# Kernel optimization log

Hardware: AMD Instinct MI355X
Metric: run time of the kernel (lower is better)

## Reference

```python
import jax, jax.numpy as jnp
import numpy as np

B, S, D, H = 2, 2048, 1024, 16  # batch, seq, embed_dim, num_heads
DH = D // H                      # head dim = 64


def setup_inputs() -> dict:
    key = jax.random.key(0)
    kx, kq, kbq, kk, kbk, kv, kbv = jax.random.split(key, 7)
    scale = 1.0 / np.sqrt(D)
    return {
        "x": jax.random.normal(kx, (B, S, D), dtype=jnp.float32),
        "Wq": jax.random.normal(kq, (D, D), dtype=jnp.float32) * scale,
        "bq": jax.random.normal(kbq, (D,), dtype=jnp.float32) * 0.01,
        "Wk": jax.random.normal(kk, (D, D), dtype=jnp.float32) * scale,
        "bk": jax.random.normal(kbk, (D,), dtype=jnp.float32) * 0.01,
        "Wv": jax.random.normal(kv, (D, D), dtype=jnp.float32) * scale,
        "bv": jax.random.normal(kbv, (D,), dtype=jnp.float32) * 0.01,
    }


def reference(x, Wq, bq, Wk, bk, Wv, bv):
    # ooqkv_type == 'q', odeint_method == 'id': q branch = act(Linear(x)), exact GELU (torch nn.GELU default)
    q = jax.nn.gelu(x @ Wq + bq, approximate=False)
    k = x @ Wk + bk
    v = x @ Wv + bv
    # [B, S, D] -> [B, S, H, DH]
    q = q.reshape(B, S, H, DH)
    k = k.reshape(B, S, H, DH)
    v = v.reshape(B, S, H, DH)
    # NOTE: original module has NO 1/sqrt(d) scale — faithful reproduction
    att = jnp.einsum("bqhd,bkhd->bhqk", q, k)
    att = jax.nn.softmax(att, axis=-1)
    out = jnp.einsum("bhqk,bkhd->bqhd", att, v)
    return out.reshape(B, S, D)
```

## Files before the change

### kernel.cpp

```cpp
#include <hip/hip_runtime.h>
#include <math.h>

#define B_  2
#define S_  2048
#define D_  1024
#define H_  16
#define DH_ 64
#define M_  (B_ * S_)

typedef _Float16 half_t;
typedef __attribute__((ext_vector_type(8))) _Float16 h8;
typedef __attribute__((ext_vector_type(4))) _Float16 h4;
typedef __attribute__((ext_vector_type(4))) float   f32x4;

#define LOG2E 1.44269504088896f

__device__ __forceinline__ void gll16(const half_t* g, half_t* l) {
    __builtin_amdgcn_global_load_lds(
        (__attribute__((address_space(1))) const void*)g,
        (__attribute__((address_space(3))) void*)l, 16, 0, 0);
}

__global__ __launch_bounds__(256) void prep_k(
    const float* __restrict__ x, half_t* __restrict__ xh,
    const float* __restrict__ Wq, const float* __restrict__ Wk,
    const float* __restrict__ Wv, half_t* __restrict__ Wt)
{
    const int bx = blockIdx.x;
    if (bx < 2048) {
        const size_t i = ((size_t)bx * 256 + threadIdx.x) * 8;
        const float4 a = *(const float4*)(x + i);
        const float4 b = *(const float4*)(x + i + 4);
        h8 o;
        o[0] = (half_t)a.x; o[1] = (half_t)a.y; o[2] = (half_t)a.z; o[3] = (half_t)a.w;
        o[4] = (half_t)b.x; o[5] = (half_t)b.y; o[6] = (half_t)b.z; o[7] = (half_t)b.w;
        *(h8*)(xh + i) = o;
    } else {
        const int gb    = bx - 2048;
        const int which = gb >> 9;
        const float* __restrict__ W = (which == 0) ? Wq : (which == 1) ? Wk : Wv;
        half_t* __restrict__ T = Wt + (size_t)which * D_ * D_;
        const int gw   = (gb & 511) * 4 + (threadIdx.x >> 6);
        const int lane = threadIdx.x & 63;
        const int n    = (gw & 15) * 64 + lane;
        const int k0   = (gw >> 4) * 8;
        h8 o;
        #pragma unroll
        for (int t = 0; t < 8; ++t) o[t] = (half_t)W[(size_t)(k0 + t) * D_ + n];
        *(h8*)(T + (size_t)n * D_ + k0) = o;
    }
}

__global__ __launch_bounds__(512) void qkv_gemm_f16(
    const half_t* __restrict__ xh, const half_t* __restrict__ Wt,
    const float* __restrict__ bq, const float* __restrict__ bk,
    const float* __restrict__ bv,
    half_t* __restrict__ Qo, half_t* __restrict__ Ko, half_t* __restrict__ Vt)
{
    const int lin = blockIdx.y * 24 + blockIdx.x;
    const int swz = (lin & 7) * 96 + (lin >> 3);
    const int n0g = (swz % 24) * 128;
    const int m0  = (swz / 24) * 128;
    const int which = n0g >> 10;
    const int n0    = n0g & 1023;
    const half_t* __restrict__ Wp  = Wt + (size_t)which * D_ * D_;
    const float* __restrict__ bias = (which == 0) ? bq : (which == 1) ? bk : bv;

    const int tid = threadIdx.x, lane = tid & 63, wave = tid >> 6;
    const int wm = (wave & 3) * 32, wn = (wave >> 2) * 64;
    const int ln = lane & 15, quad = lane >> 4;

    __shared__ __align__(16) half_t SMEM[128 * 136];
    half_t* const As = SMEM;
    half_t* const Bs = SMEM + 128 * 64;

    const int r0  = tid >> 3, c0 = tid & 7;
    const int cs  = c0 ^ (r0 & 7);
    const half_t* aS = xh + (size_t)(m0 + r0) * D_ + cs * 8;
    const half_t* bS = Wp + (size_t)(n0 + r0) * D_ + cs * 8;

    f32x4 acc[2][4];
    #pragma unroll
    for (int i = 0; i < 2; ++i)
        #pragma unroll
        for (int j = 0; j < 4; ++j) acc[i][j] = (f32x4){0.f, 0.f, 0.f, 0.f};

    for (int k0 = 0; k0 < D_; k0 += 64) {
        __syncthreads();
        gll16(aS,            &As[tid * 8]);
        gll16(aS + 64 * D_,  &As[(tid + 512) * 8]);
        gll16(bS,            &Bs[tid * 8]);
        gll16(bS + 64 * D_,  &Bs[(tid + 512) * 8]);
        aS += 64; bS += 64;
        __syncthreads();

        #pragma unroll
        for (int kc = 0; kc < 2; ++kc) {
            h8 af[2], bf[4];
            #pragma unroll
            for (int i = 0; i < 2; ++i) {
                const int r = wm + i * 16 + ln;
                af[i] = *(const h8*)&As[r * 64 + (((kc << 2) + quad) ^ (r & 7)) * 8];
            }
            #pragma unroll
            for (int j = 0; j < 4; ++j) {
                const int r = wn + j * 16 + ln;
                bf[j] = *(const h8*)&Bs[r * 64 + (((kc << 2) + quad) ^ (r & 7)) * 8];
            }
            #pragma unroll
            for (int i = 0; i < 2; ++i)
                #pragma unroll
                for (int j = 0; j < 4; ++j)
                    acc[i][j] = __builtin_amdgcn_mfma_f32_16x16x32_f16(
                        af[i], bf[j], acc[i][j], 0, 0, 0);
        }
    }

    if (which == 2) {
        #pragma unroll
        for (int j = 0; j < 4; ++j) {
            const int col = n0 + wn + j * 16 + ln;
            const int h = col >> 6, d = col & 63;
            const float bb = bias[col];
            #pragma unroll
            for (int i = 0; i < 2; ++i) {
                const int sg = m0 + wm + i * 16 + quad * 4;
                const int b  = sg >> 11, srow = sg & 2047;
                h4 pv;
                #pragma unroll
                for (int r = 0; r < 4; ++r) pv[r] = (half_t)(acc[i][j][r] + bb);
                *(h4*)(Vt + (((size_t)(b * H_ + h) * DH_ + d) * S_ + srow)) = pv;
            }
        }
    } else {
        half_t* __restrict__ outp = (which == 0) ? Qo : Ko;
        __syncthreads();
        #pragma unroll
        for (int j = 0; j < 4; ++j) {
            const int col = wn + j * 16 + ln;
            const float bb = bias[n0 + col];
            #pragma unroll
            for (int i = 0; i < 2; ++i) {
                #pragma unroll
                for (int r = 0; r < 4; ++r) {
                    const int row = wm + i * 16 + quad * 4 + r;
                    float t = acc[i][j][r] + bb;
                    if (which == 0) {
                        const float u = t * fmaf(t * t, 0.0356774081f, 0.7978845608f);
                        const float e = __builtin_amdgcn_exp2f(u * -2.88539008178f);
                        t = t * __builtin_amdgcn_rcpf(1.0f + e) * LOG2E;
                    }
                    SMEM[row * 136 + col] = (half_t)t;
                }
            }
        }
        __syncthreads();
        const int cc = tid & 15;
        const int rr = tid >> 4;
        #pragma unroll
        for (int p = 0; p < 4; ++p) {
            const int row = p * 32 + rr;
            const h8 v = *(const h8*)&SMEM[row * 136 + cc * 8];
            *(h8*)(outp + (size_t)(m0 + row) * D_ + n0 + cc * 8) = v;
        }
    }
}

#define DEFER_THR 10.0f
#define ATTN_TILE(KS, VS)                                                     \
    do {                                                                      \
        f32x4 sa[4];                                                          \
        __builtin_amdgcn_s_setprio(1);                                        \
        _Pragma("unroll")                                                     \
        for (int j = 0; j < 4; ++j) {                                         \
            const int rK = j * 16 + ln;                                       \
            const h8 ka0 = *(const h8*)&KS[rK * 64 + ((quad)     ^ (rK & 7)) * 8]; \
            const h8 ka1 = *(const h8*)&KS[rK * 64 + ((quad + 4) ^ (rK & 7)) * 8]; \
            f32x4 t = (f32x4){0.f, 0.f, 0.f, 0.f};                            \
            t = __builtin_amdgcn_mfma_f32_16x16x32_f16(ka0, qa0, t, 0, 0, 0); \
            t = __builtin_amdgcn_mfma_f32_16x16x32_f16(ka1, qa1, t, 0, 0, 0); \
            sa[j] = t;                                                        \
        }                                                                     \
        __builtin_amdgcn_s_setprio(0);                                        \
        float mxa = sa[0][0];                                                 \
        _Pragma("unroll")                                                     \
        for (int j = 0; j < 4; ++j)                                           \
            _Pragma("unroll")                                                 \
            for (int r = 0; r < 4; ++r) mxa = fmaxf(mxa, sa[j][r]);           \
        mxa = fmaxf(mxa, __shfl_xor(mxa, 16, 64));                            \
        mxa = fmaxf(mxa, __shfl_xor(mxa, 32, 64));                            \
        if (__ballot(mxa > m_a + DEFER_THR)) {                                \
            const float mna = fmaxf(m_a, mxa);                                \
            const float ala = __builtin_amdgcn_exp2f(m_a - mna);              \
            m_a = mna;                                                        \
            float ra[4];                                                      \
            _Pragma("unroll")                                                 \
            for (int r = 0; r < 4; ++r) ra[r] = __shfl(ala, quad * 4 + r, 64);\
            _Pragma("unroll")                                                 \
            for (int r = 0; r < 4; ++r) {                                     \
                la[r] *= ra[r];                                               \
                _Pragma("unroll")                                             \
                for (int j = 0; j < 4; ++j) Oa[j][r] *= ra[r];                \
            }                                                                 \
        }                                                                     \
        _Pragma("unroll")                                                     \
        for (int j = 0; j < 4; ++j) {                                         \
            h4 pva;                                                           \
            _Pragma("unroll")                                                 \
            for (int r = 0; r < 4; ++r)                                       \
                pva[r] = (half_t)__builtin_amdgcn_exp2f(sa[j][r] - m_a);      \
            *(h4*)&QPs[wave * 16 + ln][j * 16 + quad * 4] = pva;              \
        }                                                                     \
        const h8 pa0 = *(const h8*)&QPs[wave * 16 + ln][quad * 8];            \
        const h8 pa1 = *(const h8*)&QPs[wave * 16 + ln][32 + quad * 8];       \
        __builtin_amdgcn_s_setprio(1);                                        \
        _Pragma("unroll")                                                     \
        for (int j = 0; j < 4; ++j) {                                         \
            const int rV = j * 16 + ln;                                       \
            const h8 vb0 = *(const h8*)&VS[rV * 64 + ((quad)     ^ (rV & 7)) * 8]; \
            const h8 vb1 = *(const h8*)&VS[rV * 64 + ((quad + 4) ^ (rV & 7)) * 8]; \
            Oa[j] = __builtin_amdgcn_mfma_f32_16x16x32_f16(pa0, vb0, Oa[j], 0, 0, 0); \
            Oa[j] = __builtin_amdgcn_mfma_f32_16x16x32_f16(pa1, vb1, Oa[j], 0, 0, 0); \
        }                                                                     \
        la = __builtin_amdgcn_mfma_f32_16x16x32_f16(pa0, ones8, la, 0, 0, 0); \
        la = __builtin_amdgcn_mfma_f32_16x16x32_f16(pa1, ones8, la, 0, 0, 0); \
        __builtin_amdgcn_s_setprio(0);                                        \
    } while (0)

__global__ __launch_bounds__(512) void attn_f16(
    const half_t* __restrict__ Q, const half_t* __restrict__ K,
    const half_t* __restrict__ Vt, float* __restrict__ out)
{
    const int tid  = threadIdx.x;
    const int lane = tid & 63;
    const int wave = tid >> 6;
    const int ln   = lane & 15;
    const int quad = lane >> 4;

    const int lin = blockIdx.y * 16 + blockIdx.x;
    const int swz = (lin & 7) * 64 + (lin >> 3);
    const int bh  = swz >> 4;
    const int b   = bh >> 4;
    const int h   = bh & 15;
    const int q0  = (swz & 15) * 128;

    const half_t* __restrict__ Qb  = Q  + (size_t)b * S_ * D_ + h * DH_;
    const half_t* __restrict__ Kb  = K  + (size_t)b * S_ * D_ + h * DH_;
    const half_t* __restrict__ Vtb = Vt + (size_t)bh * DH_ * S_;

    __shared__ __align__(16) half_t Ks0[64 * 64];
    __shared__ __align__(16) half_t Vs0[64 * 64];
    __shared__ __align__(16) half_t Ks1[64 * 64];
    __shared__ __align__(16) half_t Vs1[64 * 64];
    __shared__ __align__(16) half_t QPs[128][72];

    const int sr  = tid >> 3, sc0 = tid & 7;
    const int scs = sc0 ^ (sr & 7);
    const half_t* kS = Kb  + (size_t)sr * D_ + scs * 8;
    const half_t* vS = Vtb + (size_t)sr * S_ + scs * 8;
    half_t* const kD0 = &Ks0[tid * 8];
    half_t* const vD0 = &Vs0[tid * 8];
    half_t* const kD1 = &Ks1[tid * 8];
    half_t* const vD1 = &Vs1[tid * 8];

    gll16(kS, kD0); gll16(vS, vD0);
    kS += 64 * D_; vS += 64;

    #pragma unroll
    for (int l = 0; l < 2; ++l) {
        const int c = tid + l * 512;
        const int r = c >> 3, k8 = c & 7;
        *(h8*)&QPs[r][k8 * 8] = *(const h8*)(Qb + (size_t)(q0 + r) * D_ + k8 * 8);
    }
    __syncthreads();
    const h8 qa0 = *(const h8*)&QPs[wave * 16 + ln][quad * 8];
    const h8 qa1 = *(const h8*)&QPs[wave * 16 + ln][32 + quad * 8];

    h8 ones8;
    #pragma unroll
    for (int t = 0; t < 8; ++t) ones8[t] = (half_t)1.0f;

    f32x4 Oa[4];
    #pragma unroll
    for (int j = 0; j < 4; ++j) Oa[j] = (f32x4){0.f, 0.f, 0.f, 0.f};
    f32x4 la = (f32x4){0.f, 0.f, 0.f, 0.f};
    float m_a = -INFINITY;

    for (int it = 0; it < 16; ++it) {
        gll16(kS, kD1); gll16(vS, vD1);
        kS += 64 * D_; vS += 64;
        ATTN_TILE(Ks0, Vs0);
        __syncthreads();

        if (it < 15) {
            gll16(kS, kD0); gll16(vS, vD0);
            kS += 64 * D_; vS += 64;
        }
        ATTN_TILE(Ks1, Vs1);
        __syncthreads();
    }

    #pragma unroll
    for (int r = 0; r < 4; ++r) {
        const float iva = 1.0f / la[r];
        const int rowa = q0 + wave * 16 + quad * 4 + r;
        #pragma unroll
        for (int j = 0; j < 4; ++j)
            out[((size_t)b * S_ + rowa) * D_ + h * DH_ + j * 16 + ln] = Oa[j][r] * iva;
    }
}

extern "C" void kernel_launch(void* const* d_in, const int* in_sizes, int n_in,
                              void* d_out, int out_size, void* d_ws, size_t ws_size,
                              hipStream_t stream) {
    const float* x  = (const float*)d_in[0];
    const float* Wq = (const float*)d_in[1];
    const float* bq = (const float*)d_in[2];
    const float* Wk = (const float*)d_in[3];
    const float* bk = (const float*)d_in[4];
    const float* Wv = (const float*)d_in[5];
    const float* bv = (const float*)d_in[6];
    float* out = (float*)d_out;

    const size_t nmd = (size_t)M_ * D_;
    const size_t ndd = (size_t)D_ * D_;
    half_t* xh  = (half_t*)d_ws;
    half_t* Wt  = xh + nmd;
    half_t* Qh  = Wt + 3 * ndd;
    half_t* Kh  = Qh + nmd;
    half_t* Vtw = Kh + nmd;

    prep_k<<<2048 + 1536, 256, 0, stream>>>(x, xh, Wq, Wk, Wv, Wt);
    qkv_gemm_f16<<<dim3(3 * D_ / 128, M_ / 128), 512, 0, stream>>>(
        xh, Wt, bq, bk, bv, Qh, Kh, Vtw);
    attn_f16<<<dim3(S_ / 128, B_ * H_), 512, 0, stream>>>(Qh, Kh, Vtw, out);
}
```

Measured before the change: 168.8 us.

## Process two 16-row query tiles per wave in attention with 256-thread blocks

Each wave of the attention kernel now handles 32 query rows as two 16-row subtiles, and the block shrinks from 512 to 256 threads. Each K/V fragment read from LDS is reused for both subtiles, roughly halving LDS traffic per MFMA. The softmax statistics are tracked per subtile, and the K/V tile loads are split across fewer threads. The cost is more registers per wave and fewer waves per block to hide latency, which may lower occupancy.

```diff
diff --git a/kernel.cpp b/kernel.cpp
--- a/kernel.cpp
+++ b/kernel.cpp
@@ -169,7 +169,7 @@
 #define DEFER_THR 10.0f
 #define ATTN_TILE(KS, VS)                                                     \
     do {                                                                      \
-        f32x4 sa[4];                                                          \
+        f32x4 sa[4], sb[4];                                                   \
         __builtin_amdgcn_s_setprio(1);                                        \
         _Pragma("unroll")                                                     \
         for (int j = 0; j < 4; ++j) {                                         \
@@ -180,39 +180,60 @@
             t = __builtin_amdgcn_mfma_f32_16x16x32_f16(ka0, qa0, t, 0, 0, 0); \
             t = __builtin_amdgcn_mfma_f32_16x16x32_f16(ka1, qa1, t, 0, 0, 0); \
             sa[j] = t;                                                        \
+            f32x4 u = (f32x4){0.f, 0.f, 0.f, 0.f};                            \
+            u = __builtin_amdgcn_mfma_f32_16x16x32_f16(ka0, qc0, u, 0, 0, 0); \
+            u = __builtin_amdgcn_mfma_f32_16x16x32_f16(ka1, qc1, u, 0, 0, 0); \
+            sb[j] = u;                                                        \
         }                                                                     \
         __builtin_amdgcn_s_setprio(0);                                        \
-        float mxa = sa[0][0];                                                 \
+        float mxa = sa[0][0], mxb = sb[0][0];                                 \
         _Pragma("unroll")                                                     \
         for (int j = 0; j < 4; ++j)                                           \
             _Pragma("unroll")                                                 \
-            for (int r = 0; r < 4; ++r) mxa = fmaxf(mxa, sa[j][r]);           \
+            for (int r = 0; r < 4; ++r) {                                     \
+                mxa = fmaxf(mxa, sa[j][r]);                                   \
+                mxb = fmaxf(mxb, sb[j][r]);                                   \
+            }                                                                 \
         mxa = fmaxf(mxa, __shfl_xor(mxa, 16, 64));                            \
         mxa = fmaxf(mxa, __shfl_xor(mxa, 32, 64));                            \
-        if (__ballot(mxa > m_a + DEFER_THR)) {                                \
+        mxb = fmaxf(mxb, __shfl_xor(mxb, 16, 64));                            \
+        mxb = fmaxf(mxb, __shfl_xor(mxb, 32, 64));                            \
+        if (__ballot(mxa > m_a + DEFER_THR || mxb > m_b + DEFER_THR)) {       \
             const float mna = fmaxf(m_a, mxa);                                \
+            const float mnb = fmaxf(m_b, mxb);                                \
             const float ala = __builtin_amdgcn_exp2f(m_a - mna);              \
-            m_a = mna;                                                        \
-            float ra[4];                                                      \
-            _Pragma("unroll")                                                 \
-            for (int r = 0; r < 4; ++r) ra[r] = __shfl(ala, quad * 4 + r, 64);\
+            const float alb = __builtin_amdgcn_exp2f(m_b - mnb);              \
+            m_a = mna; m_b = mnb;                                             \
+            float ra[4], rb[4];                                               \
             _Pragma("unroll")                                                 \
             for (int r = 0; r < 4; ++r) {                                     \
-                la[r] *= ra[r];                                               \
+                ra[r] = __shfl(ala, quad * 4 + r, 64);                        \
+                rb[r] = __shfl(alb, quad * 4 + r, 64);                        \
+            }                                                                 \
+            _Pragma("unroll")                                                 \
+            for (int r = 0; r < 4; ++r) {                                     \
+                la[r] *= ra[r]; lb[r] *= rb[r];                               \
                 _Pragma("unroll")                                             \
-                for (int j = 0; j < 4; ++j) Oa[j][r] *= ra[r];                \
+                for (int j = 0; j < 4; ++j) {                                 \
+                    Oa[j][r] *= ra[r]; Ob[j][r] *= rb[r];                     \
+                }                                                             \
             }                                                                 \
         }                                                                     \
         _Pragma("unroll")                                                     \
         for (int j = 0; j < 4; ++j) {                                         \
-            h4 pva;                                                           \
+            h4 pva, pvb;                                                      \
             _Pragma("unroll")                                                 \
-            for (int r = 0; r < 4; ++r)                                       \
+            for (int r = 0; r < 4; ++r) {                                     \
                 pva[r] = (half_t)__builtin_amdgcn_exp2f(sa[j][r] - m_a);      \
-            *(h4*)&QPs[wave * 16 + ln][j * 16 + quad * 4] = pva;              \
+                pvb[r] = (half_t)__builtin_amdgcn_exp2f(sb[j][r] - m_b);      \
+            }                                                                 \
+            *(h4*)&QPs[wave * 32 + ln][j * 16 + quad * 4]      = pva;         \
+            *(h4*)&QPs[wave * 32 + 16 + ln][j * 16 + quad * 4] = pvb;         \
         }                                                                     \
-        const h8 pa0 = *(const h8*)&QPs[wave * 16 + ln][quad * 8];            \
-        const h8 pa1 = *(const h8*)&QPs[wave * 16 + ln][32 + quad * 8];       \
+        const h8 pa0 = *(const h8*)&QPs[wave * 32 + ln][quad * 8];            \
+        const h8 pa1 = *(const h8*)&QPs[wave * 32 + ln][32 + quad * 8];       \
+        const h8 pb0 = *(const h8*)&QPs[wave * 32 + 16 + ln][quad * 8];       \
+        const h8 pb1 = *(const h8*)&QPs[wave * 32 + 16 + ln][32 + quad * 8];  \
         __builtin_amdgcn_s_setprio(1);                                        \
         _Pragma("unroll")                                                     \
         for (int j = 0; j < 4; ++j) {                                         \
@@ -221,13 +242,17 @@
             const h8 vb1 = *(const h8*)&VS[rV * 64 + ((quad + 4) ^ (rV & 7)) * 8]; \
             Oa[j] = __builtin_amdgcn_mfma_f32_16x16x32_f16(pa0, vb0, Oa[j], 0, 0, 0); \
             Oa[j] = __builtin_amdgcn_mfma_f32_16x16x32_f16(pa1, vb1, Oa[j], 0, 0, 0); \
+            Ob[j] = __builtin_amdgcn_mfma_f32_16x16x32_f16(pb0, vb0, Ob[j], 0, 0, 0); \
+            Ob[j] = __builtin_amdgcn_mfma_f32_16x16x32_f16(pb1, vb1, Ob[j], 0, 0, 0); \
         }                                                                     \
         la = __builtin_amdgcn_mfma_f32_16x16x32_f16(pa0, ones8, la, 0, 0, 0); \
         la = __builtin_amdgcn_mfma_f32_16x16x32_f16(pa1, ones8, la, 0, 0, 0); \
+        lb = __builtin_amdgcn_mfma_f32_16x16x32_f16(pb0, ones8, lb, 0, 0, 0); \
+        lb = __builtin_amdgcn_mfma_f32_16x16x32_f16(pb1, ones8, lb, 0, 0, 0); \
         __builtin_amdgcn_s_setprio(0);                                        \
     } while (0)
 
-__global__ __launch_bounds__(512) void attn_f16(
+__global__ __launch_bounds__(256) void attn_f16(
     const half_t* __restrict__ Q, const half_t* __restrict__ K,
     const half_t* __restrict__ Vt, float* __restrict__ out)
 {
@@ -258,42 +283,53 @@
     const int scs = sc0 ^ (sr & 7);
     const half_t* kS = Kb  + (size_t)sr * D_ + scs * 8;
     const half_t* vS = Vtb + (size_t)sr * S_ + scs * 8;
-    half_t* const kD0 = &Ks0[tid * 8];
-    half_t* const vD0 = &Vs0[tid * 8];
-    half_t* const kD1 = &Ks1[tid * 8];
-    half_t* const vD1 = &Vs1[tid * 8];
-
-    gll16(kS, kD0); gll16(vS, vD0);
+
+    gll16(kS,           &Ks0[tid * 8]);
+    gll16(kS + 32 * D_, &Ks0[(tid + 256) * 8]);
+    gll16(vS,           &Vs0[tid * 8]);
+    gll16(vS + 32 * S_, &Vs0[(tid + 256) * 8]);
     kS += 64 * D_; vS += 64;
 
     #pragma unroll
-    for (int l = 0; l < 2; ++l) {
-        const int c = tid + l * 512;
+    for (int l = 0; l < 4; ++l) {
+        const int c = tid + l * 256;
         const int r = c >> 3, k8 = c & 7;
         *(h8*)&QPs[r][k8 * 8] = *(const h8*)(Qb + (size_t)(q0 + r) * D_ + k8 * 8);
     }
     __syncthreads();
-    const h8 qa0 = *(const h8*)&QPs[wave * 16 + ln][quad * 8];
-    const h8 qa1 = *(const h8*)&QPs[wave * 16 + ln][32 + quad * 8];
+    const h8 qa0 = *(const h8*)&QPs[wave * 32 + ln][quad * 8];
+    const h8 qa1 = *(const h8*)&QPs[wave * 32 + ln][32 + quad * 8];
+    const h8 qc0 = *(const h8*)&QPs[wave * 32 + 16 + ln][quad * 8];
+    const h8 qc1 = *(const h8*)&QPs[wave * 32 + 16 + ln][32 + quad * 8];
 
     h8 ones8;
     #pragma unroll
     for (int t = 0; t < 8; ++t) ones8[t] = (half_t)1.0f;
 
-    f32x4 Oa[4];
-    #pragma unroll
-    for (int j = 0; j < 4; ++j) Oa[j] = (f32x4){0.f, 0.f, 0.f, 0.f};
+    f32x4 Oa[4], Ob[4];
+    #pragma unroll
+    for (int j = 0; j < 4; ++j) {
+        Oa[j] = (f32x4){0.f, 0.f, 0.f, 0.f};
+        Ob[j] = (f32x4){0.f, 0.f, 0.f, 0.f};
+    }
     f32x4 la = (f32x4){0.f, 0.f, 0.f, 0.f};
-    float m_a = -INFINITY;
+    f32x4 lb = (f32x4){0.f, 0.f, 0.f, 0.f};
+    float m_a = -INFINITY, m_b = -INFINITY;
 
     for (int it = 0; it < 16; ++it) {
-        gll16(kS, kD1); gll16(vS, vD1);
+        gll16(kS,           &Ks1[tid * 8]);
+        gll16(kS + 32 * D_, &Ks1[(tid + 256) * 8]);
+        gll16(vS,           &Vs1[tid * 8]);
+        gll16(vS + 32 * S_, &Vs1[(tid + 256) * 8]);
         kS += 64 * D_; vS += 64;
         ATTN_TILE(Ks0, Vs0);
         __syncthreads();
 
         if (it < 15) {
-            gll16(kS, kD0); gll16(vS, vD0);
+            gll16(kS,           &Ks0[tid * 8]);
+            gll16(kS + 32 * D_, &Ks0[(tid + 256) * 8]);
+            gll16(vS,           &Vs0[tid * 8]);
+            gll16(vS + 32 * S_, &Vs0[(tid + 256) * 8]);
             kS += 64 * D_; vS += 64;
         }
         ATTN_TILE(Ks1, Vs1);
@@ -303,10 +339,14 @@
     #pragma unroll
     for (int r = 0; r < 4; ++r) {
         const float iva = 1.0f / la[r];
-        const int rowa = q0 + wave * 16 + quad * 4 + r;
-        #pragma unroll
-        for (int j = 0; j < 4; ++j)
+        const float ivb = 1.0f / lb[r];
+        const int rowa = q0 + wave * 32 + quad * 4 + r;
+        const int rowb = rowa + 16;
+        #pragma unroll
+        for (int j = 0; j < 4; ++j) {
             out[((size_t)b * S_ + rowa) * D_ + h * DH_ + j * 16 + ln] = Oa[j][r] * iva;
+            out[((size_t)b * S_ + rowb) * D_ + h * DH_ + j * 16 + ln] = Ob[j][r] * ivb;
+        }
     }
 }
 
@@ -333,5 +373,5 @@
     prep_k<<<2048 + 1536, 256, 0, stream>>>(x, xh, Wq, Wk, Wv, Wt);
     qkv_gemm_f16<<<dim3(3 * D_ / 128, M_ / 128), 512, 0, stream>>>(
         xh, Wt, bq, bk, bv, Qh, Kh, Vtw);
-    attn_f16<<<dim3(S_ / 128, B_ * H_), 512, 0, stream>>>(Qh, Kh, Vtw, out);
-}
+    attn_f16<<<dim3(S_ / 128, B_ * H_), 256, 0, stream>>>(Qh, Kh, Vtw, out);
+}
```

Measured after the change: 190.3 us. 1.13x slower.
